# Performance work log

Hardware: AMD Instinct MI355X
Metric: run time of the kernel (lower is better)

## Reference

```python
import jax, jax.numpy as jnp
import numpy as np

B, T, D, H = 8, 2048, 1024, 64

def setup_inputs() -> dict:
    key = jax.random.key(0)
    k1, k2, k3, k4 = jax.random.split(key, 4)
    x = jax.random.normal(k1, (B, T, D), dtype=jnp.float32)
    s = 1.0 / np.sqrt(D)
    Wq = jax.random.normal(k2, (D, H), dtype=jnp.float32) * s
    Wk = jax.random.normal(k3, (D, H), dtype=jnp.float32) * s
    Wv = jax.random.normal(k4, (D, H), dtype=jnp.float32) * s
    return {"x": x, "Wq": Wq, "Wk": Wk, "Wv": Wv}

def reference(x, Wq, Wk, Wv):
    q = jnp.einsum('btd,dh->bth', x, Wq)
    k = jnp.einsum('btd,dh->bth', x, Wk)
    v = jnp.einsum('btd,dh->bth', x, Wv)
    scores = jnp.einsum('bqh,bkh->bqk', q, k) / jnp.sqrt(jnp.float32(H))
    Tq = x.shape[1]
    causal = jnp.tril(jnp.ones((Tq, Tq), dtype=bool))
    scores = jnp.where(causal, scores, -jnp.inf)
    w = jax.nn.softmax(scores, axis=-1)
    return jnp.einsum('bqk,bkh->bqh', w, v)
```

## Files before the change

kernel.cpp:

```cpp
#include <hip/hip_runtime.h>
#include <cstddef>

typedef _Float16 half8 __attribute__((ext_vector_type(8)));
typedef __fp16 fp16x2 __attribute__((ext_vector_type(2)));
typedef float f32x4 __attribute__((ext_vector_type(4)));

#define WT_OFF 0
#define Q_OFF  393216
#define K_OFF  2490368
#define V_OFF  4587520

__device__ __forceinline__ void glds16(const void* g, const void* l) {
  __builtin_amdgcn_global_load_lds(
      (const __attribute__((address_space(1))) unsigned*)g,
      (__attribute__((address_space(3))) unsigned*)l, 16, 0, 0);
}

__global__ __launch_bounds__(256) void wcvt_kernel(const float* __restrict__ wq,
                                                   const float* __restrict__ wk,
                                                   const float* __restrict__ wv,
                                                   _Float16* __restrict__ wt) {
  int i = blockIdx.x * 256 + threadIdx.x;
  int d = i >> 6;
  int c = i & 63;
  wt[(size_t)c * 1024 + d] = (_Float16)wq[i];
  wt[(size_t)(64 + c) * 1024 + d] = (_Float16)wk[i];
  wt[(size_t)(128 + c) * 1024 + d] = (_Float16)wv[i];
}

__global__ __launch_bounds__(256, 2) void qkv_kernel(const float* __restrict__ x,
                                                     const _Float16* __restrict__ wt,
                                                     _Float16* __restrict__ qws,
                                                     _Float16* __restrict__ kws,
                                                     _Float16* __restrict__ vtws) {
  __shared__ __align__(16) float As[32 * 64];
  __shared__ __align__(16) _Float16 Bs[192 * 64];
  const int tid = threadIdx.x;
  const int wave = tid >> 6;
  const int lane = tid & 63;
  const int quad = lane >> 4;
  const int ln = lane & 15;
  const int t0 = blockIdx.x * 32;

  f32x4 acc[2][3];
#pragma unroll
  for (int mt = 0; mt < 2; ++mt)
#pragma unroll
    for (int nt = 0; nt < 3; ++nt) acc[mt][nt] = (f32x4){0.f, 0.f, 0.f, 0.f};

  int aU[2], aRow[2], aC[2];
#pragma unroll
  for (int i = 0; i < 2; ++i) {
    aU[i] = (i * 4 + wave) * 64 + lane;
    aRow[i] = aU[i] >> 4;
    aC[i] = (aU[i] & 15) ^ (aRow[i] & 15);
  }
  int bU[6], bN[6], bS8[6];
#pragma unroll
  for (int i = 0; i < 6; ++i) {
    bU[i] = (i * 4 + wave) * 64 + lane;
    bN[i] = bU[i] >> 3;
    bS8[i] = (bU[i] & 7) ^ (bN[i] & 7);
  }

  for (int kc = 0; kc < 16; ++kc) {
#pragma unroll
    for (int i = 0; i < 2; ++i)
      glds16(x + (size_t)(t0 + aRow[i]) * 1024 + kc * 64 + aC[i] * 4,
             &As[((i * 4 + wave) * 64) * 4]);
#pragma unroll
    for (int i = 0; i < 6; ++i)
      glds16(wt + (size_t)bN[i] * 1024 + kc * 64 + bS8[i] * 8,
             &Bs[((i * 4 + wave) * 64) * 8]);
    __syncthreads();

#pragma unroll
    for (int s = 0; s < 2; ++s) {
      half8 av[2];
#pragma unroll
      for (int mt = 0; mt < 2; ++mt) {
        const int r = mt * 16 + ln;
        const int c0 = s * 8 + quad * 2;
        f32x4 u0 = *(const f32x4*)&As[(r * 16 + (c0 ^ ln)) * 4];
        f32x4 u1 = *(const f32x4*)&As[(r * 16 + ((c0 + 1) ^ ln)) * 4];
        union { fp16x2 p[4]; half8 v; } a;
        a.p[0] = __builtin_amdgcn_cvt_pkrtz(u0[0], u0[1]);
        a.p[1] = __builtin_amdgcn_cvt_pkrtz(u0[2], u0[3]);
        a.p[2] = __builtin_amdgcn_cvt_pkrtz(u1[0], u1[1]);
        a.p[3] = __builtin_amdgcn_cvt_pkrtz(u1[2], u1[3]);
        av[mt] = a.v;
      }
#pragma unroll
      for (int nt = 0; nt < 3; ++nt) {
        const int n = wave * 48 + nt * 16 + ln;
        const int s8 = s * 4 + quad;
        half8 b = *(const half8*)&Bs[(n * 8 + (s8 ^ (ln & 7))) * 8];
#pragma unroll
        for (int mt = 0; mt < 2; ++mt)
          acc[mt][nt] = __builtin_amdgcn_mfma_f32_16x16x32_f16(av[mt], b, acc[mt][nt], 0, 0, 0);
      }
    }
    __syncthreads();
  }

#pragma unroll
  for (int mt = 0; mt < 2; ++mt) {
    const int trow0 = t0 + mt * 16 + quad * 4;
#pragma unroll
    for (int nt = 0; nt < 3; ++nt) {
      const int c = wave * 48 + nt * 16 + ln;
      const f32x4 a = acc[mt][nt];
      if (c < 64) {
#pragma unroll
        for (int r = 0; r < 4; ++r)
          qws[(size_t)(trow0 + r) * 64 + c] = (_Float16)(a[r] * 0.18033688011112042f);
      } else if (c < 128) {
#pragma unroll
        for (int r = 0; r < 4; ++r) {
          const int t = trow0 + r;
          const int pos = (t & ~31) | (((t & 31) >> 1) + ((t & 1) << 4));
          kws[(size_t)pos * 64 + (c - 64)] = (_Float16)a[r];
        }
      } else {
        const int h = c - 128;
        const int bb = trow0 >> 11;
        const int ti = trow0 & 2047;
        union { _Float16 h4[4]; short4 s; } u;
#pragma unroll
        for (int r = 0; r < 4; ++r) u.h4[r] = (_Float16)a[r];
        *(short4*)&vtws[(size_t)(bb * 64 + h) * 2048 + ti] = u.s;
      }
    }
  }
}

__global__ __launch_bounds__(256) void attn_kernel(const _Float16* __restrict__ qws,
                                                   const _Float16* __restrict__ kws,
                                                   const _Float16* __restrict__ vtws,
                                                   float* __restrict__ out) {
  __shared__ __align__(16) _Float16 Ks[2][64 * 64];
  __shared__ __align__(16) _Float16 Vs[2][64 * 64];
  __shared__ __align__(16) _Float16 plds[4 * 16 * 40];
  __shared__ __align__(16) float Olds[2][16 * 64];
  __shared__ float llds[2][16];

  const int tid = threadIdx.x;
  const int wave = tid >> 6;
  const int lane = tid & 63;
  const int quad = lane >> 4;
  const int ln = lane & 15;
  const int b = blockIdx.x & 7;
  const int pr = blockIdx.x >> 3;
  const size_t bb = (size_t)b * 2048;
  const int qt = wave >> 1;
  const int kh = wave & 1;
  _Float16* myp = plds + wave * 640;

  const float NEG_INF = -__builtin_inff();

  int kR[2], kC8[2], vH[2], vC8[2];
#pragma unroll
  for (int i = 0; i < 2; ++i) {
    const int u = i * 256 + wave * 64 + lane;
    kR[i] = u >> 3;
    kC8[i] = (u & 7) ^ (kR[i] & 7);
    vH[i] = u >> 3;
    vC8[i] = (u & 7) ^ (vH[i] & 7);
  }

  for (int pass = 0; pass < 2; ++pass) {
    const int t = (pass == 0) ? (63 - pr) : pr;
    const int t0 = t * 32;
    const int nch = (32 * t + 95) >> 6;

    const _Float16* qrow = qws + (bb + t0 + qt * 16 + ln) * 64;
    const half8 qf0 = *(const half8*)(qrow + quad * 8);
    const half8 qf1 = *(const half8*)(qrow + 32 + quad * 8);

    float l[4] = {0.f, 0.f, 0.f, 0.f};
    f32x4 O[4];
#pragma unroll
    for (int h = 0; h < 4; ++h) O[h] = (f32x4){0.f, 0.f, 0.f, 0.f};

#pragma unroll
    for (int i = 0; i < 2; ++i) {
      glds16(kws + (bb + kR[i]) * 64 + kC8[i] * 8,
             &Ks[0][(i * 256 + wave * 64) * 8]);
      glds16(vtws + (size_t)(b * 64 + vH[i]) * 2048 + vC8[i] * 8,
             &Vs[0][(i * 256 + wave * 64) * 8]);
    }
    __syncthreads();

    for (int c = 0; c < nch; ++c) {
      const int k0 = c * 64;
      const int buf = c & 1;
      if (c + 1 < nch) {
        const int nk0 = k0 + 64;
        const int nb = (c + 1) & 1;
#pragma unroll
        for (int i = 0; i < 2; ++i) {
          glds16(kws + (bb + nk0 + kR[i]) * 64 + kC8[i] * 8,
                 &Ks[nb][(i * 256 + wave * 64) * 8]);
          glds16(vtws + (size_t)(b * 64 + vH[i]) * 2048 + nk0 + vC8[i] * 8,
                 &Vs[nb][(i * 256 + wave * 64) * 8]);
        }
      }

      const int rb = kh * 32 + ln;
      half8 kf00 = *(const half8*)&Ks[buf][(rb * 8 + ((0 + quad) ^ (ln & 7))) * 8];
      half8 kf01 = *(const half8*)&Ks[buf][(rb * 8 + ((4 + quad) ^ (ln & 7))) * 8];
      half8 kf10 = *(const half8*)&Ks[buf][((rb + 16) * 8 + ((0 + quad) ^ (ln & 7))) * 8];
      half8 kf11 = *(const half8*)&Ks[buf][((rb + 16) * 8 + ((4 + quad) ^ (ln & 7))) * 8];

      f32x4 S0 = (f32x4){0.f, 0.f, 0.f, 0.f};
      f32x4 S1 = (f32x4){0.f, 0.f, 0.f, 0.f};
      S0 = __builtin_amdgcn_mfma_f32_16x16x32_f16(qf0, kf00, S0, 0, 0, 0);
      S0 = __builtin_amdgcn_mfma_f32_16x16x32_f16(qf1, kf01, S0, 0, 0, 0);
      S1 = __builtin_amdgcn_mfma_f32_16x16x32_f16(qf0, kf10, S1, 0, 0, 0);
      S1 = __builtin_amdgcn_mfma_f32_16x16x32_f16(qf1, kf11, S1, 0, 0, 0);

      const int k0c = k0 + kh * 32;
      if (k0c + 31 > t0 + qt * 16) {
        const int key0 = k0c + 2 * ln;
#pragma unroll
        for (int r = 0; r < 4; ++r) {
          const int tq = t0 + qt * 16 + quad * 4 + r;
          if (key0 > tq) S0[r] = NEG_INF;
          if (key0 + 1 > tq) S1[r] = NEG_INF;
        }
      }

#pragma unroll
      for (int r = 0; r < 4; ++r) {
        const float p0 = exp2f(S0[r] - 12.f);
        const float p1 = exp2f(S1[r] - 12.f);
        l[r] += p0 + p1;
        union { fp16x2 v; unsigned u; } pk;
        pk.v = __builtin_amdgcn_cvt_pkrtz(p0, p1);
        *(unsigned*)&myp[(quad * 4 + r) * 40 + 2 * ln] = pk.u;
      }

      half8 pfr = *(const half8*)(myp + ln * 40 + quad * 8);
#pragma unroll
      for (int ht = 0; ht < 4; ++ht) {
        const int h = ht * 16 + ln;
        half8 vf = *(const half8*)&Vs[buf][(h * 8 + ((kh * 4 + quad) ^ (ln & 7))) * 8];
        O[ht] = __builtin_amdgcn_mfma_f32_16x16x32_f16(pfr, vf, O[ht], 0, 0, 0);
      }
      __syncthreads();
    }

#pragma unroll
    for (int r = 0; r < 4; ++r) {
      l[r] += __shfl_xor(l[r], 1);
      l[r] += __shfl_xor(l[r], 2);
      l[r] += __shfl_xor(l[r], 4);
      l[r] += __shfl_xor(l[r], 8);
    }

    if (kh == 1) {
#pragma unroll
      for (int r = 0; r < 4; ++r) {
        const int row = quad * 4 + r;
        if (ln == 0) llds[qt][row] = l[r];
#pragma unroll
        for (int ht = 0; ht < 4; ++ht)
          Olds[qt][row * 64 + ht * 16 + ln] = O[ht][r];
      }
    }
    __syncthreads();
    if (kh == 0) {
#pragma unroll
      for (int r = 0; r < 4; ++r) {
        const int row = quad * 4 + r;
        const float inv = 1.0f / (l[r] + llds[qt][row]);
        float* orow = out + (bb + t0 + qt * 16 + row) * 64;
#pragma unroll
        for (int ht = 0; ht < 4; ++ht)
          orow[ht * 16 + ln] = (O[ht][r] + Olds[qt][row * 64 + ht * 16 + ln]) * inv;
      }
    }
    __syncthreads();
  }
}

extern "C" void kernel_launch(void* const* d_in, const int* in_sizes, int n_in,
                              void* d_out, int out_size, void* d_ws, size_t ws_size,
                              hipStream_t stream) {
  const float* x  = (const float*)d_in[0];
  const float* wq = (const float*)d_in[1];
  const float* wk = (const float*)d_in[2];
  const float* wv = (const float*)d_in[3];

  char* ws = (char*)d_ws;
  _Float16* wt   = (_Float16*)(ws + WT_OFF);
  _Float16* qws  = (_Float16*)(ws + Q_OFF);
  _Float16* kws  = (_Float16*)(ws + K_OFF);
  _Float16* vtws = (_Float16*)(ws + V_OFF);
  float* outp = (float*)d_out;

  wcvt_kernel<<<256, 256, 0, stream>>>(wq, wk, wv, wt);
  qkv_kernel<<<512, 256, 0, stream>>>(x, wt, qws, kws, vtws);
  attn_kernel<<<256, 256, 0, stream>>>(qws, kws, vtws, outp);
}
```

Measured before the change: 148.1 us.

## Double-buffer QKV projection, split attention into one tile per block, coalesce weight convert

The QKV projection kernel now double-buffers its x and weight tiles in LDS, so the next K-chunk's async global-to-LDS loads overlap the MFMA work on the current chunk. The attention kernel drops the paired two-pass tile scheme: it launches 512 blocks, one query tile each, ordered heaviest first, with launch bounds requesting 2 blocks per CU. The weight-conversion kernel is re-indexed so its fp16 writes are coalesced, at the cost of strided fp32 reads. In exchange, the projection kernel doubles its LDS footprint, and load balancing across the causal tiles now depends on the hardware block scheduler rather than explicit pairing.

```diff
diff --git a/kernel.cpp b/kernel.cpp
--- a/kernel.cpp
+++ b/kernel.cpp
@@ -20,12 +20,14 @@
                                                    const float* __restrict__ wk,
                                                    const float* __restrict__ wv,
                                                    _Float16* __restrict__ wt) {
-  int i = blockIdx.x * 256 + threadIdx.x;
-  int d = i >> 6;
-  int c = i & 63;
-  wt[(size_t)c * 1024 + d] = (_Float16)wq[i];
-  wt[(size_t)(64 + c) * 1024 + d] = (_Float16)wk[i];
-  wt[(size_t)(128 + c) * 1024 + d] = (_Float16)wv[i];
+  int idx = blockIdx.x * 256 + threadIdx.x;
+  int c = idx >> 10;
+  int d = idx & 1023;
+  float v;
+  if (c < 64)       v = wq[d * 64 + c];
+  else if (c < 128) v = wk[d * 64 + (c - 64)];
+  else              v = wv[d * 64 + (c - 128)];
+  wt[idx] = (_Float16)v;
 }
 
 __global__ __launch_bounds__(256, 2) void qkv_kernel(const float* __restrict__ x,
@@ -33,8 +35,8 @@
                                                      _Float16* __restrict__ qws,
                                                      _Float16* __restrict__ kws,
                                                      _Float16* __restrict__ vtws) {
-  __shared__ __align__(16) float As[32 * 64];
-  __shared__ __align__(16) _Float16 Bs[192 * 64];
+  __shared__ __align__(16) float As[2][32 * 64];
+  __shared__ __align__(16) _Float16 Bs[2][192 * 64];
   const int tid = threadIdx.x;
   const int wave = tid >> 6;
   const int lane = tid & 63;
@@ -48,31 +50,42 @@
 #pragma unroll
     for (int nt = 0; nt < 3; ++nt) acc[mt][nt] = (f32x4){0.f, 0.f, 0.f, 0.f};
 
-  int aU[2], aRow[2], aC[2];
+  int aRow[2], aC[2];
 #pragma unroll
   for (int i = 0; i < 2; ++i) {
-    aU[i] = (i * 4 + wave) * 64 + lane;
-    aRow[i] = aU[i] >> 4;
-    aC[i] = (aU[i] & 15) ^ (aRow[i] & 15);
-  }
-  int bU[6], bN[6], bS8[6];
+    const int u = (i * 4 + wave) * 64 + lane;
+    aRow[i] = u >> 4;
+    aC[i] = (u & 15) ^ (aRow[i] & 15);
+  }
+  int bN[6], bS8[6];
 #pragma unroll
   for (int i = 0; i < 6; ++i) {
-    bU[i] = (i * 4 + wave) * 64 + lane;
-    bN[i] = bU[i] >> 3;
-    bS8[i] = (bU[i] & 7) ^ (bN[i] & 7);
-  }
+    const int u = (i * 4 + wave) * 64 + lane;
+    bN[i] = u >> 3;
+    bS8[i] = (u & 7) ^ (bN[i] & 7);
+  }
+
+#pragma unroll
+  for (int i = 0; i < 2; ++i)
+    glds16(x + (size_t)(t0 + aRow[i]) * 1024 + aC[i] * 4, &As[0][((i * 4 + wave) * 64) * 4]);
+#pragma unroll
+  for (int i = 0; i < 6; ++i)
+    glds16(wt + (size_t)bN[i] * 1024 + bS8[i] * 8, &Bs[0][((i * 4 + wave) * 64) * 8]);
+  __syncthreads();
 
   for (int kc = 0; kc < 16; ++kc) {
-#pragma unroll
-    for (int i = 0; i < 2; ++i)
-      glds16(x + (size_t)(t0 + aRow[i]) * 1024 + kc * 64 + aC[i] * 4,
-             &As[((i * 4 + wave) * 64) * 4]);
-#pragma unroll
-    for (int i = 0; i < 6; ++i)
-      glds16(wt + (size_t)bN[i] * 1024 + kc * 64 + bS8[i] * 8,
-             &Bs[((i * 4 + wave) * 64) * 8]);
-    __syncthreads();
+    const int buf = kc & 1;
+    if (kc + 1 < 16) {
+      const int nb = buf ^ 1;
+#pragma unroll
+      for (int i = 0; i < 2; ++i)
+        glds16(x + (size_t)(t0 + aRow[i]) * 1024 + (kc + 1) * 64 + aC[i] * 4,
+               &As[nb][((i * 4 + wave) * 64) * 4]);
+#pragma unroll
+      for (int i = 0; i < 6; ++i)
+        glds16(wt + (size_t)bN[i] * 1024 + (kc + 1) * 64 + bS8[i] * 8,
+               &Bs[nb][((i * 4 + wave) * 64) * 8]);
+    }
 
 #pragma unroll
     for (int s = 0; s < 2; ++s) {
@@ -81,8 +94,8 @@
       for (int mt = 0; mt < 2; ++mt) {
         const int r = mt * 16 + ln;
         const int c0 = s * 8 + quad * 2;
-        f32x4 u0 = *(const f32x4*)&As[(r * 16 + (c0 ^ ln)) * 4];
-        f32x4 u1 = *(const f32x4*)&As[(r * 16 + ((c0 + 1) ^ ln)) * 4];
+        f32x4 u0 = *(const f32x4*)&As[buf][(r * 16 + (c0 ^ ln)) * 4];
+        f32x4 u1 = *(const f32x4*)&As[buf][(r * 16 + ((c0 + 1) ^ ln)) * 4];
         union { fp16x2 p[4]; half8 v; } a;
         a.p[0] = __builtin_amdgcn_cvt_pkrtz(u0[0], u0[1]);
         a.p[1] = __builtin_amdgcn_cvt_pkrtz(u0[2], u0[3]);
@@ -94,7 +107,7 @@
       for (int nt = 0; nt < 3; ++nt) {
         const int n = wave * 48 + nt * 16 + ln;
         const int s8 = s * 4 + quad;
-        half8 b = *(const half8*)&Bs[(n * 8 + (s8 ^ (ln & 7))) * 8];
+        half8 b = *(const half8*)&Bs[buf][(n * 8 + (s8 ^ (ln & 7))) * 8];
 #pragma unroll
         for (int mt = 0; mt < 2; ++mt)
           acc[mt][nt] = __builtin_amdgcn_mfma_f32_16x16x32_f16(av[mt], b, acc[mt][nt], 0, 0, 0);
@@ -123,21 +136,21 @@
         }
       } else {
         const int h = c - 128;
-        const int bb = trow0 >> 11;
+        const int bbb = trow0 >> 11;
         const int ti = trow0 & 2047;
         union { _Float16 h4[4]; short4 s; } u;
 #pragma unroll
         for (int r = 0; r < 4; ++r) u.h4[r] = (_Float16)a[r];
-        *(short4*)&vtws[(size_t)(bb * 64 + h) * 2048 + ti] = u.s;
-      }
-    }
-  }
-}
-
-__global__ __launch_bounds__(256) void attn_kernel(const _Float16* __restrict__ qws,
-                                                   const _Float16* __restrict__ kws,
-                                                   const _Float16* __restrict__ vtws,
-                                                   float* __restrict__ out) {
+        *(short4*)&vtws[(size_t)(bbb * 64 + h) * 2048 + ti] = u.s;
+      }
+    }
+  }
+}
+
+__global__ __launch_bounds__(256, 2) void attn_kernel(const _Float16* __restrict__ qws,
+                                                      const _Float16* __restrict__ kws,
+                                                      const _Float16* __restrict__ vtws,
+                                                      float* __restrict__ out) {
   __shared__ __align__(16) _Float16 Ks[2][64 * 64];
   __shared__ __align__(16) _Float16 Vs[2][64 * 64];
   __shared__ __align__(16) _Float16 plds[4 * 16 * 40];
@@ -150,7 +163,8 @@
   const int quad = lane >> 4;
   const int ln = lane & 15;
   const int b = blockIdx.x & 7;
-  const int pr = blockIdx.x >> 3;
+  const int tile = 63 - (blockIdx.x >> 3);
+  const int t0 = tile * 32;
   const size_t bb = (size_t)b * 2048;
   const int qt = wave >> 1;
   const int kh = wave & 1;
@@ -158,129 +172,120 @@
 
   const float NEG_INF = -__builtin_inff();
 
-  int kR[2], kC8[2], vH[2], vC8[2];
+  int sR[2], sC8[2];
 #pragma unroll
   for (int i = 0; i < 2; ++i) {
     const int u = i * 256 + wave * 64 + lane;
-    kR[i] = u >> 3;
-    kC8[i] = (u & 7) ^ (kR[i] & 7);
-    vH[i] = u >> 3;
-    vC8[i] = (u & 7) ^ (vH[i] & 7);
-  }
-
-  for (int pass = 0; pass < 2; ++pass) {
-    const int t = (pass == 0) ? (63 - pr) : pr;
-    const int t0 = t * 32;
-    const int nch = (32 * t + 95) >> 6;
-
-    const _Float16* qrow = qws + (bb + t0 + qt * 16 + ln) * 64;
-    const half8 qf0 = *(const half8*)(qrow + quad * 8);
-    const half8 qf1 = *(const half8*)(qrow + 32 + quad * 8);
-
-    float l[4] = {0.f, 0.f, 0.f, 0.f};
-    f32x4 O[4];
-#pragma unroll
-    for (int h = 0; h < 4; ++h) O[h] = (f32x4){0.f, 0.f, 0.f, 0.f};
-
-#pragma unroll
-    for (int i = 0; i < 2; ++i) {
-      glds16(kws + (bb + kR[i]) * 64 + kC8[i] * 8,
-             &Ks[0][(i * 256 + wave * 64) * 8]);
-      glds16(vtws + (size_t)(b * 64 + vH[i]) * 2048 + vC8[i] * 8,
-             &Vs[0][(i * 256 + wave * 64) * 8]);
+    sR[i] = u >> 3;
+    sC8[i] = (u & 7) ^ (sR[i] & 7);
+  }
+
+  const int nch = (t0 + 95) >> 6;
+
+  const _Float16* qrow = qws + (bb + t0 + qt * 16 + ln) * 64;
+  const half8 qf0 = *(const half8*)(qrow + quad * 8);
+  const half8 qf1 = *(const half8*)(qrow + 32 + quad * 8);
+
+  float l[4] = {0.f, 0.f, 0.f, 0.f};
+  f32x4 O[4];
+#pragma unroll
+  for (int h = 0; h < 4; ++h) O[h] = (f32x4){0.f, 0.f, 0.f, 0.f};
+
+#pragma unroll
+  for (int i = 0; i < 2; ++i) {
+    glds16(kws + (bb + sR[i]) * 64 + sC8[i] * 8, &Ks[0][(i * 256 + wave * 64) * 8]);
+    glds16(vtws + (size_t)(b * 64 + sR[i]) * 2048 + sC8[i] * 8,
+           &Vs[0][(i * 256 + wave * 64) * 8]);
+  }
+  __syncthreads();
+
+  for (int c = 0; c < nch; ++c) {
+    const int k0 = c * 64;
+    const int buf = c & 1;
+    if (c + 1 < nch) {
+      const int nb = buf ^ 1;
+#pragma unroll
+      for (int i = 0; i < 2; ++i) {
+        glds16(kws + (bb + k0 + 64 + sR[i]) * 64 + sC8[i] * 8,
+               &Ks[nb][(i * 256 + wave * 64) * 8]);
+        glds16(vtws + (size_t)(b * 64 + sR[i]) * 2048 + k0 + 64 + sC8[i] * 8,
+               &Vs[nb][(i * 256 + wave * 64) * 8]);
+      }
+    }
+
+    const int rb = kh * 32 + ln;
+    half8 kf00 = *(const half8*)&Ks[buf][(rb * 8 + ((0 + quad) ^ (ln & 7))) * 8];
+    half8 kf01 = *(const half8*)&Ks[buf][(rb * 8 + ((4 + quad) ^ (ln & 7))) * 8];
+    half8 kf10 = *(const half8*)&Ks[buf][((rb + 16) * 8 + ((0 + quad) ^ (ln & 7))) * 8];
+    half8 kf11 = *(const half8*)&Ks[buf][((rb + 16) * 8 + ((4 + quad) ^ (ln & 7))) * 8];
+
+    f32x4 S0 = (f32x4){0.f, 0.f, 0.f, 0.f};
+    f32x4 S1 = (f32x4){0.f, 0.f, 0.f, 0.f};
+    S0 = __builtin_amdgcn_mfma_f32_16x16x32_f16(qf0, kf00, S0, 0, 0, 0);
+    S0 = __builtin_amdgcn_mfma_f32_16x16x32_f16(qf1, kf01, S0, 0, 0, 0);
+    S1 = __builtin_amdgcn_mfma_f32_16x16x32_f16(qf0, kf10, S1, 0, 0, 0);
+    S1 = __builtin_amdgcn_mfma_f32_16x16x32_f16(qf1, kf11, S1, 0, 0, 0);
+
+    const int k0c = k0 + kh * 32;
+    if (k0c + 31 > t0 + qt * 16) {
+      const int key0 = k0c + 2 * ln;
+#pragma unroll
+      for (int r = 0; r < 4; ++r) {
+        const int tq = t0 + qt * 16 + quad * 4 + r;
+        if (key0 > tq) S0[r] = NEG_INF;
+        if (key0 + 1 > tq) S1[r] = NEG_INF;
+      }
+    }
+
+#pragma unroll
+    for (int r = 0; r < 4; ++r) {
+      const float p0 = exp2f(S0[r] - 12.f);
+      const float p1 = exp2f(S1[r] - 12.f);
+      l[r] += p0 + p1;
+      union { fp16x2 v; unsigned u; } pk;
+      pk.v = __builtin_amdgcn_cvt_pkrtz(p0, p1);
+      *(unsigned*)&myp[(quad * 4 + r) * 40 + 2 * ln] = pk.u;
+    }
+
+    half8 pfr = *(const half8*)(myp + ln * 40 + quad * 8);
+#pragma unroll
+    for (int ht = 0; ht < 4; ++ht) {
+      const int h = ht * 16 + ln;
+      half8 vf = *(const half8*)&Vs[buf][(h * 8 + ((kh * 4 + quad) ^ (h & 7))) * 8];
+      O[ht] = __builtin_amdgcn_mfma_f32_16x16x32_f16(pfr, vf, O[ht], 0, 0, 0);
     }
     __syncthreads();
-
-    for (int c = 0; c < nch; ++c) {
-      const int k0 = c * 64;
-      const int buf = c & 1;
-      if (c + 1 < nch) {
-        const int nk0 = k0 + 64;
-        const int nb = (c + 1) & 1;
-#pragma unroll
-        for (int i = 0; i < 2; ++i) {
-          glds16(kws + (bb + nk0 + kR[i]) * 64 + kC8[i] * 8,
-                 &Ks[nb][(i * 256 + wave * 64) * 8]);
-          glds16(vtws + (size_t)(b * 64 + vH[i]) * 2048 + nk0 + vC8[i] * 8,
-                 &Vs[nb][(i * 256 + wave * 64) * 8]);
-        }
-      }
-
-      const int rb = kh * 32 + ln;
-      half8 kf00 = *(const half8*)&Ks[buf][(rb * 8 + ((0 + quad) ^ (ln & 7))) * 8];
-      half8 kf01 = *(const half8*)&Ks[buf][(rb * 8 + ((4 + quad) ^ (ln & 7))) * 8];
-      half8 kf10 = *(const half8*)&Ks[buf][((rb + 16) * 8 + ((0 + quad) ^ (ln & 7))) * 8];
-      half8 kf11 = *(const half8*)&Ks[buf][((rb + 16) * 8 + ((4 + quad) ^ (ln & 7))) * 8];
-
-      f32x4 S0 = (f32x4){0.f, 0.f, 0.f, 0.f};
-      f32x4 S1 = (f32x4){0.f, 0.f, 0.f, 0.f};
-      S0 = __builtin_amdgcn_mfma_f32_16x16x32_f16(qf0, kf00, S0, 0, 0, 0);
-      S0 = __builtin_amdgcn_mfma_f32_16x16x32_f16(qf1, kf01, S0, 0, 0, 0);
-      S1 = __builtin_amdgcn_mfma_f32_16x16x32_f16(qf0, kf10, S1, 0, 0, 0);
-      S1 = __builtin_amdgcn_mfma_f32_16x16x32_f16(qf1, kf11, S1, 0, 0, 0);
-
-      const int k0c = k0 + kh * 32;
-      if (k0c + 31 > t0 + qt * 16) {
-        const int key0 = k0c + 2 * ln;
-#pragma unroll
-        for (int r = 0; r < 4; ++r) {
-          const int tq = t0 + qt * 16 + quad * 4 + r;
-          if (key0 > tq) S0[r] = NEG_INF;
-          if (key0 + 1 > tq) S1[r] = NEG_INF;
-        }
-      }
-
-#pragma unroll
-      for (int r = 0; r < 4; ++r) {
-        const float p0 = exp2f(S0[r] - 12.f);
-        const float p1 = exp2f(S1[r] - 12.f);
-        l[r] += p0 + p1;
-        union { fp16x2 v; unsigned u; } pk;
-        pk.v = __builtin_amdgcn_cvt_pkrtz(p0, p1);
-        *(unsigned*)&myp[(quad * 4 + r) * 40 + 2 * ln] = pk.u;
-      }
-
-      half8 pfr = *(const half8*)(myp + ln * 40 + quad * 8);
-#pragma unroll
-      for (int ht = 0; ht < 4; ++ht) {
-        const int h = ht * 16 + ln;
-        half8 vf = *(const half8*)&Vs[buf][(h * 8 + ((kh * 4 + quad) ^ (ln & 7))) * 8];
-        O[ht] = __builtin_amdgcn_mfma_f32_16x16x32_f16(pfr, vf, O[ht], 0, 0, 0);
-      }
-      __syncthreads();
-    }
-
+  }
+
+#pragma unroll
+  for (int r = 0; r < 4; ++r) {
+    l[r] += __shfl_xor(l[r], 1);
+    l[r] += __shfl_xor(l[r], 2);
+    l[r] += __shfl_xor(l[r], 4);
+    l[r] += __shfl_xor(l[r], 8);
+  }
+
+  if (kh == 1) {
 #pragma unroll
     for (int r = 0; r < 4; ++r) {
-      l[r] += __shfl_xor(l[r], 1);
-      l[r] += __shfl_xor(l[r], 2);
-      l[r] += __shfl_xor(l[r], 4);
-      l[r] += __shfl_xor(l[r], 8);
-    }
-
-    if (kh == 1) {
-#pragma unroll
-      for (int r = 0; r < 4; ++r) {
-        const int row = quad * 4 + r;
-        if (ln == 0) llds[qt][row] = l[r];
-#pragma unroll
-        for (int ht = 0; ht < 4; ++ht)
-          Olds[qt][row * 64 + ht * 16 + ln] = O[ht][r];
-      }
-    }
-    __syncthreads();
-    if (kh == 0) {
-#pragma unroll
-      for (int r = 0; r < 4; ++r) {
-        const int row = quad * 4 + r;
-        const float inv = 1.0f / (l[r] + llds[qt][row]);
-        float* orow = out + (bb + t0 + qt * 16 + row) * 64;
-#pragma unroll
-        for (int ht = 0; ht < 4; ++ht)
-          orow[ht * 16 + ln] = (O[ht][r] + Olds[qt][row * 64 + ht * 16 + ln]) * inv;
-      }
-    }
-    __syncthreads();
+      const int row = quad * 4 + r;
+      if (ln == 0) llds[qt][row] = l[r];
+#pragma unroll
+      for (int ht = 0; ht < 4; ++ht)
+        Olds[qt][row * 64 + ht * 16 + ln] = O[ht][r];
+    }
+  }
+  __syncthreads();
+  if (kh == 0) {
+#pragma unroll
+    for (int r = 0; r < 4; ++r) {
+      const int row = quad * 4 + r;
+      const float inv = 1.0f / (l[r] + llds[qt][row]);
+      float* orow = out + (bb + t0 + qt * 16 + row) * 64;
+#pragma unroll
+      for (int ht = 0; ht < 4; ++ht)
+        orow[ht * 16 + ln] = (O[ht][r] + Olds[qt][row * 64 + ht * 16 + ln]) * inv;
+    }
   }
 }
 
@@ -299,7 +304,7 @@
   _Float16* vtws = (_Float16*)(ws + V_OFF);
   float* outp = (float*)d_out;
 
-  wcvt_kernel<<<256, 256, 0, stream>>>(wq, wk, wv, wt);
+  wcvt_kernel<<<768, 256, 0, stream>>>(wq, wk, wv, wt);
   qkv_kernel<<<512, 256, 0, stream>>>(x, wt, qws, kws, vtws);
-  attn_kernel<<<256, 256, 0, stream>>>(qws, kws, vtws, outp);
-}
+  attn_kernel<<<512, 256, 0, stream>>>(qws, kws, vtws, outp);
+}
```

Result: faster. 140.9 us (-4.9%).
